# Optimization experiments

Measured on AMD Instinct MI355X. Metric: run time of the kernel, lower is better.

## Reference

```python
import jax, jax.numpy as jnp
import numpy as np

D_MODEL = 1024
N_HEADS = 16
HEAD_DIM = D_MODEL // N_HEADS


def setup_inputs() -> dict:
    key = jax.random.key(0)
    ks = jax.random.split(key, 9)
    B, T = 4, 2048
    s = 1.0 / np.sqrt(D_MODEL)
    inp = {
        'x': jax.random.normal(ks[0], (B, T, D_MODEL), jnp.float32),
        'W_q': jax.random.normal(ks[1], (D_MODEL, D_MODEL), jnp.float32) * s,
        'b_q': jnp.zeros((D_MODEL,), jnp.float32),
        'W_k': jax.random.normal(ks[2], (D_MODEL, D_MODEL), jnp.float32) * s,
        'b_k': jnp.zeros((D_MODEL,), jnp.float32),
        'W_v': jax.random.normal(ks[3], (D_MODEL, D_MODEL), jnp.float32) * s,
        'b_v': jnp.zeros((D_MODEL,), jnp.float32),
        'W_o': jax.random.normal(ks[4], (D_MODEL, D_MODEL), jnp.float32) * s,
        'b_o': jnp.zeros((D_MODEL,), jnp.float32),
    }
    return inp


def reference(x, W_q, b_q, W_k, b_k, W_v, b_v, W_o, b_o):
    B, T, _ = x.shape
    # torch Linear: y = x @ W.T + b
    def proj(W, b):
        y = jnp.einsum('btd,ed->bte', x, W) + b
        return y.reshape(B, T, N_HEADS, HEAD_DIM).transpose(0, 2, 1, 3)  # (B,H,T,hd)
    Q = proj(W_q, b_q)
    K = proj(W_k, b_k)
    V = proj(W_v, b_v)
    scores = jnp.einsum('bhqd,bhkd->bhqk', Q, K) / np.sqrt(HEAD_DIM)
    causal = jnp.tril(jnp.ones((T, T), bool))
    scores = jnp.where(causal[None, None, :, :], scores, -jnp.inf)
    attn = jax.nn.softmax(scores, axis=-1)  # dropout = identity (eval)
    out = jnp.einsum('bhqk,bhkd->bhqd', attn, V)
    out = out.transpose(0, 2, 1, 3).reshape(B, T, D_MODEL)
    return jnp.einsum('btd,ed->bte', out, W_o) + b_o
```

## Files before the change

kernel.cpp:

```cpp
#include <hip/hip_runtime.h>
#include <hip/hip_bf16.h>

#define D_MODEL 1024
#define T_SEQ   2048
#define BATCH   4
#define NHEADS  16
#define HDIM    64
#define M_ROWS  (BATCH * T_SEQ)
#define QSCALE  (0.125f * 1.44269504088896340736f)

typedef unsigned short ushortT;
typedef __attribute__((ext_vector_type(4))) float f32x4;
typedef __attribute__((ext_vector_type(8))) short s16x8;

#define GP(p) ((const __attribute__((address_space(1))) void*)(p))
#define LP(p) ((__attribute__((address_space(3))) void*)(p))

static __device__ __forceinline__ ushortT f2b(float f) {
    union { float f; unsigned u; } v; v.f = f;
    unsigned r = v.u + 0x7fffu + ((v.u >> 16) & 1u);
    return (ushortT)(r >> 16);
}

__global__ void cast_f32_bf16_swz(const float* __restrict__ src, ushortT* __restrict__ dst, int n8) {
    int i = blockIdx.x * 256 + threadIdx.x;
    if (i >= n8) return;
    const float4* s = (const float4*)src;
    float4 a = s[i * 2], b = s[i * 2 + 1];
    s16x8 r;
    r[0] = f2b(a.x); r[1] = f2b(a.y); r[2] = f2b(a.z); r[3] = f2b(a.w);
    r[4] = f2b(b.x); r[5] = f2b(b.y); r[6] = f2b(b.z); r[7] = f2b(b.w);
    ((s16x8*)dst)[i ^ ((i >> 7) & 7)] = r;
}


#define GEMM_PREAMBLE()                                                  \
    const int tid  = threadIdx.x;                                        \
    const int wave = tid >> 6, lane = tid & 63;                          \
    const int wm = wave >> 1, wn = wave & 1;                             \
    const int lr = lane & 15, lh = lane >> 4;                            \
    const int srow = tid >> 3;                                           \
    const int sg   = tid & 7;                                            \
    f32x4 acc[4][4] = {};                                                \
    const ushortT* Ag = A  + (size_t)(m0 + srow) * 1024 + sg * 8;        \
    const ushortT* Bg = Bw + (size_t)(n0 + srow) * 1024 + sg * 8;

#define STAGE_G(buf, k0)                                                               \
    do {                                                                               \
        _Pragma("unroll")                                                              \
        for (int is = 0; is < 4; ++is) {                                               \
            __builtin_amdgcn_global_load_lds(GP(Ag + (size_t)(is * 32) * 1024 + (k0)), \
                                             LP(&As[buf][is * 2048 + tid * 8]), 16, 0, 0); \
            __builtin_amdgcn_global_load_lds(GP(Bg + (size_t)(is * 32) * 1024 + (k0)), \
                                             LP(&Bs[buf][is * 2048 + tid * 8]), 16, 0, 0); \
        }                                                                              \
    } while (0)

#define COMPUTE_G(buf)                                                                 \
    do {                                                                               \
        _Pragma("unroll")                                                              \
        for (int kk = 0; kk < 2; ++kk) {                                               \
            s16x8 af[4], bfr[4];                                                       \
            const int g = ((kk * 4 + lh) ^ (lr & 7)) * 8;                              \
            _Pragma("unroll")                                                          \
            for (int i = 0; i < 4; ++i)                                                \
                af[i] = *(const s16x8*)&As[buf][(wm * 64 + i * 16 + lr) * 64 + g];     \
            _Pragma("unroll")                                                          \
            for (int j = 0; j < 4; ++j)                                                \
                bfr[j] = *(const s16x8*)&Bs[buf][(wn * 64 + j * 16 + lr) * 64 + g];    \
            __builtin_amdgcn_s_setprio(1);                                             \
            _Pragma("unroll")                                                          \
            for (int i = 0; i < 4; ++i)                                                \
                _Pragma("unroll")                                                      \
                for (int j = 0; j < 4; ++j)                                            \
                    acc[i][j] = __builtin_amdgcn_mfma_f32_16x16x32_bf16(af[i], bfr[j], acc[i][j], 0, 0, 0); \
            __builtin_amdgcn_s_setprio(0);                                             \
        }                                                                              \
    } while (0)

#define GEMM_KLOOP()                        \
    STAGE_G(0, 0);                          \
    __syncthreads();                        \
    for (int t = 0; t < 15; ++t) {          \
        const int cur = t & 1;              \
        STAGE_G(cur ^ 1, (t + 1) * 64);     \
        COMPUTE_G(cur);                     \
        __syncthreads();                    \
    }                                       \
    COMPUTE_G(1);

__global__ __launch_bounds__(256, 2) void qkv_gemm(
    const ushortT* __restrict__ A,
    const ushortT* __restrict__ Wq, const ushortT* __restrict__ Wk, const ushortT* __restrict__ Wv,
    const float* __restrict__ bq, const float* __restrict__ bk, const float* __restrict__ bv,
    ushortT* __restrict__ Qb, ushortT* __restrict__ Kb, ushortT* __restrict__ Vtb)
{
    __shared__ __attribute__((aligned(16))) ushortT As[2][128 * 64];
    __shared__ __attribute__((aligned(16))) ushortT Bs[2][128 * 64];

    const int seg = blockIdx.y >> 3;
    const int m0 = blockIdx.x * 128, n0 = (blockIdx.y & 7) * 128;
    const ushortT* Bw   = (seg == 0) ? Wq : (seg == 1) ? Wk : Wv;
    const float*   bias = (seg == 0) ? bq : (seg == 1) ? bk : bv;
    const float    scale = (seg == 0) ? QSCALE : 1.0f;

    GEMM_PREAMBLE();
    GEMM_KLOOP();

    ushortT* outp = (seg == 0) ? Qb : (seg == 1) ? Kb : Vtb;
    #pragma unroll
    for (int i = 0; i < 4; ++i) {
        #pragma unroll
        for (int j = 0; j < 4; ++j) {
            const int c = n0 + wn * 64 + j * 16 + lr;
            const float bv_ = bias[c];
            #pragma unroll
            for (int e = 0; e < 4; ++e) {
                const int r = m0 + wm * 64 + i * 16 + lh * 4 + e;
                const float val = (acc[i][j][e] + bv_) * scale;
                const int b = r >> 11, t = r & 2047;
                const int h = c >> 6,  d = c & 63;
                size_t idx;
                if (seg == 2)      idx = ((size_t)(b * NHEADS + h) * HDIM + d) * T_SEQ + (t ^ ((d & 7) << 3));
                else if (seg == 1) idx = ((size_t)(b * NHEADS + h) * T_SEQ + t) * HDIM + (d ^ ((t & 7) << 3));
                else               idx = ((size_t)(b * NHEADS + h) * T_SEQ + t) * HDIM + d;
                outp[idx] = f2b(val);
            }
        }
    }
}

__global__ __launch_bounds__(256, 2) void out_gemm(
    const ushortT* __restrict__ A, const ushortT* __restrict__ Bw,
    const float* __restrict__ bias, float* __restrict__ outp)
{
    __shared__ __attribute__((aligned(16))) ushortT As[2][128 * 64];
    __shared__ __attribute__((aligned(16))) ushortT Bs[2][128 * 64];

    const int m0 = blockIdx.x * 128, n0 = blockIdx.y * 128;

    GEMM_PREAMBLE();
    GEMM_KLOOP();

    #pragma unroll
    for (int i = 0; i < 4; ++i) {
        #pragma unroll
        for (int j = 0; j < 4; ++j) {
            const int c = n0 + wn * 64 + j * 16 + lr;
            const float bv_ = bias[c];
            #pragma unroll
            for (int e = 0; e < 4; ++e) {
                const int r = m0 + wm * 64 + i * 16 + lh * 4 + e;
                outp[(size_t)r * 1024 + c] = acc[i][j][e] + bv_;
            }
        }
    }
}

__global__ __launch_bounds__(256, 4) void attn_fwd(
    const ushortT* __restrict__ Qb, const ushortT* __restrict__ Kb,
    const ushortT* __restrict__ Vt, ushortT* __restrict__ Ob)
{
    __shared__ __attribute__((aligned(16))) ushortT Ks[2][64 * 64];
    __shared__ __attribute__((aligned(16))) ushortT Vs[2][64 * 64];
    __shared__ __attribute__((aligned(16))) ushortT Ps[4][16 * 64];

    const int tid = threadIdx.x;
    const int w = tid >> 6, lane = tid & 63;
    const int lr = lane & 15, lh = lane >> 4;

    const int blk = blockIdx.x;
    const int j   = blk >> 3;
    const int bh  = (blk & 7) * 8 + (j >> 5);
    const int qt  = 31 - (j & 31);
    const int q0  = qt * 64;

    const ushortT* qrow = Qb + ((size_t)bh * T_SEQ + q0 + w * 16 + lr) * HDIM;
    const s16x8 qf0 = *(const s16x8*)(qrow + lh * 8);
    const s16x8 qf1 = *(const s16x8*)(qrow + 32 + lh * 8);

    float m_r = -1e30f, l_r = 0.f;
    f32x4 o[4] = {};

    const int srow = tid >> 3;
    const int sk   = (tid & 7) * 8;

    const ushortT* Kbh = Kb + (size_t)bh * T_SEQ * HDIM;
    const ushortT* Vbh = Vt + (size_t)bh * HDIM * T_SEQ;

    #define STAGE(buf, kt_) do { \
        const int k0_ = (kt_) * 64; \
        const ushortT* kg = Kbh + (size_t)(k0_ + srow) * HDIM + sk; \
        const ushortT* vg = Vbh + (size_t)srow * T_SEQ + k0_ + sk; \
        __builtin_amdgcn_global_load_lds(GP(kg),                 LP(&Ks[buf][srow * 64 + sk]),        16, 0, 0); \
        __builtin_amdgcn_global_load_lds(GP(kg + 32 * HDIM),     LP(&Ks[buf][(32 + srow) * 64 + sk]), 16, 0, 0); \
        __builtin_amdgcn_global_load_lds(GP(vg),                 LP(&Vs[buf][srow * 64 + sk]),        16, 0, 0); \
        __builtin_amdgcn_global_load_lds(GP(vg + 32 * T_SEQ),    LP(&Vs[buf][(32 + srow) * 64 + sk]), 16, 0, 0); \
    } while (0)

    STAGE(0, 0);
    __syncthreads();

    const int g0 = (lh       ^ (lr & 7)) * 8;
    const int g1 = ((4 + lh) ^ (lr & 7)) * 8;

    for (int kt = 0; kt <= qt; ++kt) {
        const int cur = kt & 1;
        if (kt < qt) STAGE(cur ^ 1, kt + 1);

        f32x4 s[4];
        __builtin_amdgcn_s_setprio(1);
        #pragma unroll
        for (int ni = 0; ni < 4; ++ni) {
            const int rr = ni * 16 + lr;
            s16x8 b0 = *(const s16x8*)&Ks[cur][rr * 64 + g0];
            s16x8 b1 = *(const s16x8*)&Ks[cur][rr * 64 + g1];
            f32x4 t = {};
            t = __builtin_amdgcn_mfma_f32_16x16x32_bf16(b0, qf0, t, 0, 0, 0);
            t = __builtin_amdgcn_mfma_f32_16x16x32_bf16(b1, qf1, t, 0, 0, 0);
            s[ni] = t;
        }
        __builtin_amdgcn_s_setprio(0);

        if (kt == qt) {
            #pragma unroll
            for (int ni = 0; ni < 4; ++ni)
                #pragma unroll
                for (int e = 0; e < 4; ++e)
                    if (ni * 16 + lh * 4 + e > w * 16 + lr) s[ni][e] = -1e30f;
        }

        float pm = -1e30f;
        #pragma unroll
        for (int ni = 0; ni < 4; ++ni)
            #pragma unroll
            for (int e = 0; e < 4; ++e)
                pm = fmaxf(pm, s[ni][e]);
        pm = fmaxf(pm, __shfl_xor(pm, 16, 64));
        pm = fmaxf(pm, __shfl_xor(pm, 32, 64));
        const float mn = fmaxf(m_r, pm);
        const float sc = exp2f(m_r - mn);
        float rs = 0.f;
        #pragma unroll
        for (int ni = 0; ni < 4; ++ni)
            #pragma unroll
            for (int e = 0; e < 4; ++e) {
                const float p = exp2f(s[ni][e] - mn);
                s[ni][e] = p;
                rs += p;
            }
        rs += __shfl_xor(rs, 16, 64);
        rs += __shfl_xor(rs, 32, 64);
        l_r = l_r * sc + rs;
        m_r = mn;
        #pragma unroll
        for (int ni = 0; ni < 4; ++ni) o[ni] *= sc;

        #pragma unroll
        for (int ni = 0; ni < 4; ++ni) {
            const unsigned u0 = (unsigned)f2b(s[ni][0]) | ((unsigned)f2b(s[ni][1]) << 16);
            const unsigned u1 = (unsigned)f2b(s[ni][2]) | ((unsigned)f2b(s[ni][3]) << 16);
            *(uint2*)&Ps[w][lr * 64 + ((ni * 16 + lh * 4) ^ ((lr & 7) << 3))] = make_uint2(u0, u1);
        }
        __asm__ volatile("s_waitcnt lgkmcnt(0)" ::: "memory");
        __builtin_amdgcn_sched_barrier(0);
        const s16x8 pf0 = *(const s16x8*)&Ps[w][lr * 64 + g0];
        const s16x8 pf1 = *(const s16x8*)&Ps[w][lr * 64 + g1];

        __builtin_amdgcn_s_setprio(1);
        #pragma unroll
        for (int ni = 0; ni < 4; ++ni) {
            const int dd = ni * 16 + lr;
            s16x8 v0 = *(const s16x8*)&Vs[cur][dd * 64 + g0];
            s16x8 v1 = *(const s16x8*)&Vs[cur][dd * 64 + g1];
            o[ni] = __builtin_amdgcn_mfma_f32_16x16x32_bf16(v0, pf0, o[ni], 0, 0, 0);
            o[ni] = __builtin_amdgcn_mfma_f32_16x16x32_bf16(v1, pf1, o[ni], 0, 0, 0);
        }
        __builtin_amdgcn_s_setprio(0);
        __syncthreads();
    }

    const int b = bh >> 4, h = bh & 15;
    const int t = q0 + w * 16 + lr;
    const float inv = 1.f / l_r;
    const size_t base = ((size_t)(b * T_SEQ) + t) * D_MODEL;
    #pragma unroll
    for (int ni = 0; ni < 4; ++ni) {
        const unsigned u0 = (unsigned)f2b(o[ni][0] * inv) | ((unsigned)f2b(o[ni][1] * inv) << 16);
        const unsigned u1 = (unsigned)f2b(o[ni][2] * inv) | ((unsigned)f2b(o[ni][3] * inv) << 16);
        const int c = h * HDIM + ni * 16 + lh * 4;
        *(uint2*)&Ob[base + (c ^ ((t & 7) << 3))] = make_uint2(u0, u1);
    }
}

extern "C" void kernel_launch(void* const* d_in, const int* in_sizes, int n_in,
                              void* d_out, int out_size, void* d_ws, size_t ws_size,
                              hipStream_t stream) {
    const float* x  = (const float*)d_in[0];
    const float* Wq = (const float*)d_in[1];
    const float* bq = (const float*)d_in[2];
    const float* Wk = (const float*)d_in[3];
    const float* bk = (const float*)d_in[4];
    const float* Wv = (const float*)d_in[5];
    const float* bv = (const float*)d_in[6];
    const float* Wo = (const float*)d_in[7];
    const float* bo = (const float*)d_in[8];

    ushortT* xb  = (ushortT*)d_ws;
    ushortT* Wqb = xb  + (size_t)M_ROWS * D_MODEL;
    ushortT* Wkb = Wqb + (size_t)D_MODEL * D_MODEL;
    ushortT* Wvb = Wkb + (size_t)D_MODEL * D_MODEL;
    ushortT* Wob = Wvb + (size_t)D_MODEL * D_MODEL;
    ushortT* Qb  = Wob + (size_t)D_MODEL * D_MODEL;
    ushortT* Kb  = Qb  + (size_t)M_ROWS * D_MODEL;
    ushortT* Vtb = Kb  + (size_t)M_ROWS * D_MODEL;
    ushortT* Ob  = Vtb + (size_t)M_ROWS * D_MODEL;

    cast_f32_bf16_swz<<<4096, 256, 0, stream>>>(x,  xb,  M_ROWS * D_MODEL / 8);
    cast_f32_bf16_swz<<<512,  256, 0, stream>>>(Wq, Wqb, D_MODEL * D_MODEL / 8);
    cast_f32_bf16_swz<<<512,  256, 0, stream>>>(Wk, Wkb, D_MODEL * D_MODEL / 8);
    cast_f32_bf16_swz<<<512,  256, 0, stream>>>(Wv, Wvb, D_MODEL * D_MODEL / 8);
    cast_f32_bf16_swz<<<512,  256, 0, stream>>>(Wo, Wob, D_MODEL * D_MODEL / 8);

    qkv_gemm<<<dim3(64, 24), 256, 0, stream>>>(xb, Wqb, Wkb, Wvb, bq, bk, bv, Qb, Kb, Vtb);

    attn_fwd<<<2048, 256, 0, stream>>>(Qb, Kb, Vtb, Ob);

    out_gemm<<<dim3(64, 8), 256, 0, stream>>>(Ob, Wob, bo, (float*)d_out);
}
```

Measured before the change: 309.5 us.

## Merge cast launches, add lazy softmax rescale, use packed bf16 conversion

The five cast kernels become one launch that picks its source buffer from the global thread index, writing into the same contiguous workspace layout. In attention, the running-max rescale of the output accumulator and row sum is skipped unless some lane's new block max exceeds the old max by more than 8 (log2 domain). Per-element bf16 rounding is replaced by the hardware v_cvt_pk_bf16_f32 instruction, and the max reduction becomes a tree. These cut launch overhead and VALU work in the softmax inner loop, at the cost of letting exponentials reach up to 2^8 before renormalisation.

```diff
diff --git a/kernel.cpp b/kernel.cpp
--- a/kernel.cpp
+++ b/kernel.cpp
@@ -22,15 +22,29 @@
     return (ushortT)(r >> 16);
 }
 
-__global__ void cast_f32_bf16_swz(const float* __restrict__ src, ushortT* __restrict__ dst, int n8) {
-    int i = blockIdx.x * 256 + threadIdx.x;
-    if (i >= n8) return;
+static __device__ __forceinline__ unsigned cvtpk(float lo, float hi) {
+    unsigned r;
+    asm("v_cvt_pk_bf16_f32 %0, %1, %2" : "=v"(r) : "v"(lo), "v"(hi));
+    return r;
+}
+
+__global__ void cast_all(const float* __restrict__ x,
+                         const float* __restrict__ Wq, const float* __restrict__ Wk,
+                         const float* __restrict__ Wv, const float* __restrict__ Wo,
+                         ushortT* __restrict__ dst) {
+    const int i = blockIdx.x * 256 + threadIdx.x;
+    const float* src; int g, ob;
+    if (i < 1048576)      { src = x;  g = i;           ob = 0; }
+    else if (i < 1179648) { src = Wq; g = i - 1048576; ob = 1048576; }
+    else if (i < 1310720) { src = Wk; g = i - 1179648; ob = 1179648; }
+    else if (i < 1441792) { src = Wv; g = i - 1310720; ob = 1310720; }
+    else                  { src = Wo; g = i - 1441792; ob = 1441792; }
     const float4* s = (const float4*)src;
-    float4 a = s[i * 2], b = s[i * 2 + 1];
+    float4 a = s[g * 2], b = s[g * 2 + 1];
     s16x8 r;
     r[0] = f2b(a.x); r[1] = f2b(a.y); r[2] = f2b(a.z); r[3] = f2b(a.w);
     r[4] = f2b(b.x); r[5] = f2b(b.y); r[6] = f2b(b.z); r[7] = f2b(b.w);
-    ((s16x8*)dst)[i ^ ((i >> 7) & 7)] = r;
+    ((s16x8*)dst)[ob + (g ^ ((g >> 7) & 7))] = r;
 }
 
 
@@ -230,36 +244,43 @@
                     if (ni * 16 + lh * 4 + e > w * 16 + lr) s[ni][e] = -1e30f;
         }
 
-        float pm = -1e30f;
-        #pragma unroll
-        for (int ni = 0; ni < 4; ++ni)
-            #pragma unroll
-            for (int e = 0; e < 4; ++e)
-                pm = fmaxf(pm, s[ni][e]);
+        float pm;
+        {
+            float a0 = fmaxf(fmaxf(s[0][0], s[0][1]), fmaxf(s[0][2], s[0][3]));
+            float a1 = fmaxf(fmaxf(s[1][0], s[1][1]), fmaxf(s[1][2], s[1][3]));
+            float a2 = fmaxf(fmaxf(s[2][0], s[2][1]), fmaxf(s[2][2], s[2][3]));
+            float a3 = fmaxf(fmaxf(s[3][0], s[3][1]), fmaxf(s[3][2], s[3][3]));
+            pm = fmaxf(fmaxf(a0, a1), fmaxf(a2, a3));
+        }
         pm = fmaxf(pm, __shfl_xor(pm, 16, 64));
         pm = fmaxf(pm, __shfl_xor(pm, 32, 64));
-        const float mn = fmaxf(m_r, pm);
-        const float sc = exp2f(m_r - mn);
+
+        if (!__all(pm - m_r <= 8.f)) {
+            const float mn = fmaxf(m_r, pm);
+            const float sc = exp2f(m_r - mn);
+            l_r *= sc;
+            #pragma unroll
+            for (int ni = 0; ni < 4; ++ni) o[ni] *= sc;
+            m_r = mn;
+        }
+
         float rs = 0.f;
         #pragma unroll
         for (int ni = 0; ni < 4; ++ni)
             #pragma unroll
             for (int e = 0; e < 4; ++e) {
-                const float p = exp2f(s[ni][e] - mn);
+                const float p = exp2f(s[ni][e] - m_r);
                 s[ni][e] = p;
                 rs += p;
             }
         rs += __shfl_xor(rs, 16, 64);
         rs += __shfl_xor(rs, 32, 64);
-        l_r = l_r * sc + rs;
-        m_r = mn;
-        #pragma unroll
-        for (int ni = 0; ni < 4; ++ni) o[ni] *= sc;
+        l_r += rs;
 
         #pragma unroll
         for (int ni = 0; ni < 4; ++ni) {
-            const unsigned u0 = (unsigned)f2b(s[ni][0]) | ((unsigned)f2b(s[ni][1]) << 16);
-            const unsigned u1 = (unsigned)f2b(s[ni][2]) | ((unsigned)f2b(s[ni][3]) << 16);
+            const unsigned u0 = cvtpk(s[ni][0], s[ni][1]);
+            const unsigned u1 = cvtpk(s[ni][2], s[ni][3]);
             *(uint2*)&Ps[w][lr * 64 + ((ni * 16 + lh * 4) ^ ((lr & 7) << 3))] = make_uint2(u0, u1);
         }
         __asm__ volatile("s_waitcnt lgkmcnt(0)" ::: "memory");
@@ -286,8 +307,8 @@
     const size_t base = ((size_t)(b * T_SEQ) + t) * D_MODEL;
     #pragma unroll
     for (int ni = 0; ni < 4; ++ni) {
-        const unsigned u0 = (unsigned)f2b(o[ni][0] * inv) | ((unsigned)f2b(o[ni][1] * inv) << 16);
-        const unsigned u1 = (unsigned)f2b(o[ni][2] * inv) | ((unsigned)f2b(o[ni][3] * inv) << 16);
+        const unsigned u0 = cvtpk(o[ni][0] * inv, o[ni][1] * inv);
+        const unsigned u1 = cvtpk(o[ni][2] * inv, o[ni][3] * inv);
         const int c = h * HDIM + ni * 16 + lh * 4;
         *(uint2*)&Ob[base + (c ^ ((t & 7) << 3))] = make_uint2(u0, u1);
     }
@@ -316,11 +337,7 @@
     ushortT* Vtb = Kb  + (size_t)M_ROWS * D_MODEL;
     ushortT* Ob  = Vtb + (size_t)M_ROWS * D_MODEL;
 
-    cast_f32_bf16_swz<<<4096, 256, 0, stream>>>(x,  xb,  M_ROWS * D_MODEL / 8);
-    cast_f32_bf16_swz<<<512,  256, 0, stream>>>(Wq, Wqb, D_MODEL * D_MODEL / 8);
-    cast_f32_bf16_swz<<<512,  256, 0, stream>>>(Wk, Wkb, D_MODEL * D_MODEL / 8);
-    cast_f32_bf16_swz<<<512,  256, 0, stream>>>(Wv, Wvb, D_MODEL * D_MODEL / 8);
-    cast_f32_bf16_swz<<<512,  256, 0, stream>>>(Wo, Wob, D_MODEL * D_MODEL / 8);
+    cast_all<<<6144, 256, 0, stream>>>(x, Wq, Wk, Wv, Wo, xb);
 
     qkv_gemm<<<dim3(64, 24), 256, 0, stream>>>(xb, Wqb, Wkb, Wvb, bq, bk, bv, Qb, Kb, Vtb);
 
```

Result: faster. 296.3 us (-4.3%).
